# Performance work log

Measured on AMD Instinct MI355X. Metric: run time of the kernel, lower is better.

The kernel has to match this reference:

```python
import jax, jax.numpy as jnp
import numpy as np

B, S, D = 2, 2048, 4096
H, KV, HD = 32, 8, 128
THETA = 10000.0


def rotate_half(x):
    x1, x2 = x[..., : HD // 2], x[..., HD // 2 :]
    return jnp.concatenate((-x2, x1), axis=-1)


def setup_inputs() -> dict:
    key = jax.random.key(0)
    ks = jax.random.split(key, 8)
    s = 1.0 / np.sqrt(D)
    return {
        "hidden_states": jax.random.normal(ks[0], (B, S, D), jnp.float32),
        "modality_indicators": jax.random.randint(ks[1], (B, S), 0, 2, jnp.int64 if jax.config.jax_enable_x64 else jnp.int32),
        "position_ids": jnp.arange(S, dtype=jnp.int32),
        "Wq": jax.random.normal(ks[2], (D, H * HD), jnp.float32) * s,
        "Wk0": jax.random.normal(ks[3], (D, KV * HD), jnp.float32) * s,
        "Wk1": jax.random.normal(ks[4], (D, KV * HD), jnp.float32) * s,
        "Wv0": jax.random.normal(ks[5], (D, KV * HD), jnp.float32) * s,
        "Wv1": jax.random.normal(ks[6], (D, KV * HD), jnp.float32) * s,
        "Wo": jax.random.normal(ks[7], (H * HD, D), jnp.float32) * s,
    }


def reference(hidden_states, modality_indicators, position_ids, Wq, Wk0, Wk1, Wv0, Wv1, Wo):
    x = hidden_states
    # Multiway (modality-routed) k/v projections: per-token select between two linears.
    sel = (modality_indicators == 1)[..., None]  # [B,S,1]
    q = x @ Wq                                   # [B,S,H*HD]
    k = jnp.where(sel, x @ Wk1, x @ Wk0)         # [B,S,KV*HD]
    v = jnp.where(sel, x @ Wv1, x @ Wv0)

    q = q.reshape(B, S, H, HD).transpose(0, 2, 1, 3)    # [B,H,S,HD]
    k = k.reshape(B, S, KV, HD).transpose(0, 2, 1, 3)   # [B,KV,S,HD]
    v = v.reshape(B, S, KV, HD).transpose(0, 2, 1, 3)

    # RoPE cache and application (emb = cat(freqs, freqs))
    inv_freq = 1.0 / (THETA ** (jnp.arange(0, HD, 2, dtype=jnp.float32) / HD))
    freqs = position_ids.astype(jnp.float32)[:, None] * inv_freq[None, :]   # [S,HD/2]
    emb = jnp.concatenate((freqs, freqs), axis=-1)                          # [S,HD]
    cos = jnp.cos(emb)[None, None, :, :]                                    # [1,1,S,HD]
    sin = jnp.sin(emb)[None, None, :, :]
    q = q * cos + rotate_half(q) * sin
    k = k * cos + rotate_half(k) * sin

    # GQA: repeat kv heads
    n_rep = H // KV
    k = jnp.repeat(k, n_rep, axis=1)  # [B,H,S,HD]
    v = jnp.repeat(v, n_rep, axis=1)

    scores = jnp.einsum("bhqd,bhkd->bhqk", q, k) / np.sqrt(HD)
    causal = jnp.tril(jnp.ones((S, S), dtype=bool))
    scores = jnp.where(causal[None, None], scores, jnp.finfo(scores.dtype).min)
    attn = jax.nn.softmax(scores, axis=-1)
    ctx = jnp.einsum("bhqk,bhkd->bhqd", attn, v)            # [B,H,S,HD]
    ctx = ctx.transpose(0, 2, 1, 3).reshape(B, S, H * HD)
    return ctx @ Wo
```

## Files before the change

### kernel.cpp

```cpp
#include <hip/hip_runtime.h>

typedef unsigned short u16;
typedef unsigned int   u32;
using bf16x8 = __attribute__((ext_vector_type(8))) __bf16;
using f32x4  = __attribute__((ext_vector_type(4))) float;
using f32x16 = __attribute__((ext_vector_type(16))) float;
using u32x4  = __attribute__((ext_vector_type(4))) unsigned int;
using ushort8 = __attribute__((ext_vector_type(8))) unsigned short;


__device__ __forceinline__ u16 f2bf(float f) {
  u32 u = __builtin_bit_cast(u32, f);
  return (u16)((u + 0x7fffu + ((u >> 16) & 1u)) >> 16);
}
__device__ __forceinline__ float bf2f(u16 h) {
  return __builtin_bit_cast(float, (u32)h << 16);
}
__device__ __forceinline__ f32x4 mfma16(bf16x8 a, bf16x8 b, f32x4 c) {
  return __builtin_amdgcn_mfma_f32_16x16x32_bf16(a, b, c, 0, 0, 0);
}
__device__ __forceinline__ f32x16 mfma32(bf16x8 a, bf16x8 b, f32x16 c) {
  return __builtin_amdgcn_mfma_f32_32x32x16_bf16(a, b, c, 0, 0, 0);
}
__device__ __forceinline__ f32x16 zero16() {
  f32x16 z;
#pragma unroll
  for (int i = 0; i < 16; ++i) z[i] = 0.f;
  return z;
}
__device__ __forceinline__ void g2l16(const void* gp, void* lp) {
  __builtin_amdgcn_global_load_lds(
      (__attribute__((address_space(1))) void*)(void*)gp,
      (__attribute__((address_space(3))) void*)lp, 16, 0, 0);
}

__global__ void k_cvt(const float* __restrict__ in, u16* __restrict__ out, int n4) {
  int i = blockIdx.x * 256 + threadIdx.x;
  if (i >= n4) return;
  float4 v = ((const float4*)in)[i];
  ushort4 o;
  o.x = f2bf(v.x); o.y = f2bf(v.y); o.z = f2bf(v.z); o.w = f2bf(v.w);
  ((ushort4*)out)[i] = o;
}

__device__ __forceinline__ void tcvt_tile(const float* __restrict__ in, u16* __restrict__ out,
                                          int K, int N, int nt, int kt, u16 (*t)[72]) {
  const int n0 = nt * 64, k0 = kt * 64;
  const int tid = threadIdx.x;
  const int r = tid >> 2, c4 = (tid & 3) * 16;
  const float* src = in + (size_t)(k0 + r) * N + n0 + c4;
#pragma unroll
  for (int q = 0; q < 4; ++q) {
    float4 v = *(const float4*)(src + 4 * q);
    t[c4 + 4 * q + 0][r] = f2bf(v.x);
    t[c4 + 4 * q + 1][r] = f2bf(v.y);
    t[c4 + 4 * q + 2][r] = f2bf(v.z);
    t[c4 + 4 * q + 3][r] = f2bf(v.w);
  }
  __syncthreads();
  u16* dst = out + (size_t)(n0 + r) * K + k0 + c4;
#pragma unroll
  for (int hh = 0; hh < 2; ++hh)
    *(ushort8*)(dst + 8 * hh) = *(const ushort8*)(&t[r][c4 + 8 * hh]);
}

__global__ __launch_bounds__(256) void k_tcvt(const float* __restrict__ in, u16* __restrict__ out,
                                              int K, int N) {
  __shared__ u16 t[64][72];
  tcvt_tile(in, out, K, N, blockIdx.x, blockIdx.y, t);
}

__global__ __launch_bounds__(256) void k_tcvt5(const float* __restrict__ Wq, const float* __restrict__ Wk0,
                                               const float* __restrict__ Wv0, const float* __restrict__ Wk1,
                                               const float* __restrict__ Wv1, u16* __restrict__ WqT,
                                               u16* __restrict__ Wkv0T, u16* __restrict__ Wkv1T) {
  __shared__ u16 t[64][72];
  int bid = blockIdx.x;
  if (bid < 4096) {
    tcvt_tile(Wq, WqT, 4096, 4096, bid & 63, bid >> 6, t);
  } else {
    int r = bid - 4096;
    int mat = r >> 10, rr = r & 1023;
    const float* src = (mat == 0) ? Wk0 : (mat == 1) ? Wv0 : (mat == 2) ? Wk1 : Wv1;
    u16* dst = (mat == 0) ? Wkv0T : (mat == 1) ? (Wkv0T + (size_t)1024 * 4096)
                                  : (mat == 2) ? Wkv1T : (Wkv1T + (size_t)1024 * 4096);
    tcvt_tile(src, dst, 4096, 1024, rr & 15, rr >> 4, t);
  }
}

__global__ void k_scan(const int* __restrict__ mod, int* __restrict__ perm, int* __restrict__ meta) {
  __shared__ int ps[1024];
  const int b = blockIdx.x, t = threadIdx.x;
  perm[b * 2304 + t] = -1;
  perm[b * 2304 + 1024 + t] = -1;
  if (t < 256) perm[b * 2304 + 2048 + t] = -1;
  const int i0 = 2 * t, i1 = 2 * t + 1;
  const int f0 = (mod[b * 2048 + i0] != 1) ? 1 : 0;
  const int f1 = (mod[b * 2048 + i1] != 1) ? 1 : 0;
  const int sum = f0 + f1;
  ps[t] = sum;
  __syncthreads();
  for (int off = 1; off < 1024; off <<= 1) {
    int v = (t >= off) ? ps[t - off] : 0;
    __syncthreads();
    ps[t] += v;
    __syncthreads();
  }
  const int total0 = ps[1023];
  const int excl = ps[t] - sum;
  const int nt0 = (total0 + 255) >> 8;
  const int off1 = nt0 * 256;
  const int s0 = f0 ? excl : off1 + (i0 - excl);
  const int s1 = f1 ? (excl + f0) : off1 + (i1 - (excl + f0));
  perm[b * 2304 + s0] = i0;
  perm[b * 2304 + s1] = i1;
  if (t == 0) { meta[b * 2] = total0; meta[b * 2 + 1] = nt0; }
}

#define BARSB() { __builtin_amdgcn_s_barrier(); __builtin_amdgcn_sched_barrier(0); }
#define VMC(N)  asm volatile("s_waitcnt vmcnt(" #N ")" ::: "memory")

#define READ_A(MH, SL) { _Pragma("unroll") for (int mf_ = 0; mf_ < 4; ++mf_) {       \
    const char* a_ = (const char*)lds8 + (SL)*65536 + (MH)*16384 + (arow + mf_*16)*128; \
    afr[mf_][0] = *(const bf16x8*)(a_ + swc0);                                        \
    afr[mf_][1] = *(const bf16x8*)(a_ + swc1); } }

#define READ_B(NH, SL) { _Pragma("unroll") for (int nf_ = 0; nf_ < 2; ++nf_) {       \
    const char* b_ = (const char*)lds8 + (SL)*65536 + 32768 + (NH)*16384 + (brow + nf_*16)*128; \
    bfr[nf_][0] = *(const bf16x8*)(b_ + swc0);                                        \
    bfr[nf_][1] = *(const bf16x8*)(b_ + swc1); } }

#define MM16(MH, NH) { __builtin_amdgcn_s_setprio(1);                                 \
  _Pragma("unroll") for (int mf_ = 0; mf_ < 4; ++mf_)                                 \
    _Pragma("unroll") for (int nf_ = 0; nf_ < 2; ++nf_) {                             \
      acc[MH][mf_][NH][nf_] = mfma16(afr[mf_][0], bfr[nf_][0], acc[MH][mf_][NH][nf_]); \
      acc[MH][mf_][NH][nf_] = mfma16(afr[mf_][1], bfr[nf_][1], acc[MH][mf_][NH][nf_]); } \
  __builtin_amdgcn_s_setprio(0); }

#define STAGE_A(T, MH) { int ts_ = (T) < 64 ? (T) : 63;                               \
    char* d_ = (char*)lds8 + ((T)&1)*65536 + (MH)*16384 + wid*1024;                   \
    g2l16(pA0[MH] + ts_*64, d_); g2l16(pA1[MH] + ts_*64, d_ + 8192); }

#define STAGE_B(T, NH) { int ts_ = (T) < 64 ? (T) : 63;                               \
    char* d_ = (char*)lds8 + ((T)&1)*65536 + 32768 + (NH)*16384 + wid*1024;           \
    g2l16(pB0[NH] + ts_*64, d_); g2l16(pB1[NH] + ts_*64, d_ + 8192); }

#define G8_MAINLOOP()                                                                 \
  STAGE_A(0,0); STAGE_B(0,1); STAGE_A(0,1); STAGE_B(0,0);                             \
  STAGE_A(1,0); STAGE_B(1,1); STAGE_A(1,1);                                           \
  VMC(6); BARSB();                                                                    \
  for (int i_ = 0; i_ < 32; ++i_) {                                                   \
    const int ta_ = 2 * i_;                                                           \
    READ_A(0,0); READ_B(0,0); STAGE_B(ta_+1, 0); BARSB(); MM16(0,0); BARSB();         \
    READ_B(1,0);              STAGE_A(ta_+2, 0); BARSB(); MM16(0,1); BARSB();         \
    READ_A(1,0);              STAGE_B(ta_+2, 1); BARSB(); MM16(1,1); BARSB();         \
    READ_B(0,0);              STAGE_A(ta_+2, 1); BARSB(); MM16(1,0); VMC(4); BARSB(); \
    READ_A(0,1); READ_B(0,1); STAGE_B(ta_+2, 0); BARSB(); MM16(0,0); BARSB();         \
    READ_B(1,1);              STAGE_A(ta_+3, 0); BARSB(); MM16(0,1); BARSB();         \
    READ_A(1,1);              STAGE_B(ta_+3, 1); BARSB(); MM16(1,1); BARSB();         \
    READ_B(0,1);              STAGE_A(ta_+3, 1); BARSB(); MM16(1,0); VMC(4); BARSB(); \
  }

__global__ __launch_bounds__(512, 2) void k_gemm8(const u16* __restrict__ A, const u16* __restrict__ Bt,
                                                  float* __restrict__ Cp) {
  __shared__ u16 lds8[65536];
  const int tid = threadIdx.x, wid = tid >> 6, l = tid & 63, g = l >> 4, li = l & 15;
  const int wr = wid >> 2, wc = wid & 3;
  const int bid = blockIdx.x;
  const int swz = (bid & 7) * 32 + (bid >> 3);
  const int m0 = (swz >> 4) * 256, n0 = (swz & 15) * 256;

  const int swc0 = (g * 16) ^ ((li & 7) << 4);
  const int swc1 = (64 + g * 16) ^ ((li & 7) << 4);
  const int arow = wr * 64 + li;
  const int brow = wc * 32 + li;

  const int l8a = tid * 16, l8b = 8192 + tid * 16;
  const int oa = l8a ^ (((l8a >> 7) & 7) << 4), ob = l8b ^ (((l8b >> 7) & 7) << 4);
  const int rl0 = oa >> 7, cb0 = oa & 127, rl1 = ob >> 7, cb1 = ob & 127;
  const int RA0 = (rl0 >> 6) * 128 + (rl0 & 63), RA1 = (rl1 >> 6) * 128 + (rl1 & 63);
  const int CB0 = (rl0 >> 5) * 64 + (rl0 & 31), CB1 = (rl1 >> 5) * 64 + (rl1 & 31);
  const u16 *pA0[2], *pA1[2], *pB0[2], *pB1[2];
#pragma unroll
  for (int mh = 0; mh < 2; ++mh) {
    pA0[mh] = A + (size_t)(m0 + RA0 + mh * 64) * 4096 + cb0 / 2;
    pA1[mh] = A + (size_t)(m0 + RA1 + mh * 64) * 4096 + cb1 / 2;
    pB0[mh] = Bt + (size_t)(n0 + CB0 + mh * 32) * 4096 + cb0 / 2;
    pB1[mh] = Bt + (size_t)(n0 + CB1 + mh * 32) * 4096 + cb1 / 2;
  }

  bf16x8 afr[4][2], bfr[2][2];
  const f32x4 vzero = {0.f, 0.f, 0.f, 0.f};
  f32x4 acc[2][4][2][2];
#pragma unroll
  for (int a = 0; a < 2; ++a)
#pragma unroll
    for (int b = 0; b < 4; ++b)
#pragma unroll
      for (int c = 0; c < 2; ++c)
#pragma unroll
        for (int d = 0; d < 2; ++d) acc[a][b][c][d] = vzero;

  G8_MAINLOOP();

#pragma unroll
  for (int mh = 0; mh < 2; ++mh)
#pragma unroll
    for (int mf = 0; mf < 4; ++mf)
#pragma unroll
      for (int nh = 0; nh < 2; ++nh)
#pragma unroll
        for (int nf = 0; nf < 2; ++nf)
#pragma unroll
          for (int j = 0; j < 4; ++j) {
            int row = m0 + wr * 128 + mh * 64 + mf * 16 + g * 4 + j;
            int col = n0 + wc * 64 + nh * 32 + nf * 16 + li;
            Cp[(size_t)row * 4096 + col] = acc[mh][mf][nh][nf][j];
          }
}

#define TB16(T, VMLIT, DOSTAGE)                                              \
  {                                                                          \
    asm volatile("s_waitcnt vmcnt(" VMLIT ")" ::: "memory");                 \
    __builtin_amdgcn_s_barrier();                                            \
    __builtin_amdgcn_sched_barrier(0);                                       \
    const u16* base_ = lds + ((T) & 3) * 16384;                              \
    bf16x8 bfr[4], afr[4];                                                   \
    _Pragma("unroll")                                                        \
    for (int nf = 0; nf < 4; ++nf)                                           \
      bfr[nf] = *(const bf16x8*)(base_ + boff + nf * 512);                   \
    _Pragma("unroll")                                                        \
    for (int mf = 0; mf < 4; ++mf)                                           \
      afr[mf] = *(const bf16x8*)(base_ + aoff + mf * 512);                   \
    if (DOSTAGE) stage((T) + 3);                                             \
    __builtin_amdgcn_s_setprio(1);                                           \
    _Pragma("unroll")                                                        \
    for (int mf = 0; mf < 4; ++mf)                                           \
      _Pragma("unroll")                                                      \
      for (int nf = 0; nf < 4; ++nf)                                         \
        acc[mf][nf] = mfma16(afr[mf], bfr[nf], acc[mf][nf]);                 \
    __builtin_amdgcn_s_setprio(0);                                           \
  }

#define LOOP16()                                                             \
  stage(0); stage(1); stage(2);                                              \
  for (int t = 0; t < 125; ++t) TB16(t, "4", true);                          \
  TB16(125, "4", false);                                                     \
  TB16(126, "2", false);                                                     \
  TB16(127, "0", false);

__global__ __launch_bounds__(1024, 4) void k_gemmQKV(const u16* __restrict__ Xb, const u16* __restrict__ WqT,
                                                     const u16* __restrict__ B0, const u16* __restrict__ B1,
                                                     const int* __restrict__ perm, const int* __restrict__ meta,
                                                     u16* __restrict__ Qr, u16* __restrict__ Ksel,
                                                     u16* __restrict__ Vsel) {
  __shared__ u16 lds[4 * 16384];
  const int tid = threadIdx.x, wid = tid >> 6, l = tid & 63, g = l >> 4, li = l & 15;
  const int wr = wid >> 2, wc = wid & 3;
  const int bid = blockIdx.x;
  const bool isQ = bid < 256;

  const int srow = wid * 16 + (l >> 2);
  const int sgg = (l & 3) ^ ((l >> 3) & 3);

  int m0 = 0, n0 = 0, bb = 0, tm = 0;
  const u16 *pA, *pB;
  if (isQ) {
    const int swz = (bid & 7) * 32 + (bid >> 3);
    m0 = (swz >> 4) * 256; n0 = (swz & 15) * 256;
    pA = Xb + (size_t)(m0 + srow) * 4096 + sgg * 8;
    pB = WqT + (size_t)(n0 + srow) * 4096 + sgg * 8;
  } else {
    const int kb = bid - 256;
    const int seg = kb >> 3;
    n0 = (kb & 7) * 256;
    bb = seg / 9; tm = seg % 9;
    const int nt0 = meta[bb * 2 + 1];
    const u16* Bt = (tm >= nt0) ? B1 : B0;
    int t0 = perm[bb * 2304 + tm * 256 + srow];
    if (t0 < 0) t0 = 0;
    pA = Xb + ((size_t)bb * 2048 + t0) * 4096 + sgg * 8;
    pB = Bt + (size_t)(n0 + srow) * 4096 + sgg * 8;
  }

  auto stage = [&](int t) {
    u16* da = (u16*)lds + (t & 3) * 16384 + wid * 512;
    g2l16(pA + t * 32, da);
    g2l16(pB + t * 32, da + 8192);
  };

  const int lsl8 = (g ^ ((li >> 1) & 3)) * 8;
  const int aoff = (wr * 64 + li) * 32 + lsl8;
  const int boff = 8192 + (wc * 64 + li) * 32 + lsl8;

  const f32x4 vzero = {0.f, 0.f, 0.f, 0.f};
  f32x4 acc[4][4];
#pragma unroll
  for (int m = 0; m < 4; ++m)
#pragma unroll
    for (int n = 0; n < 4; ++n) acc[m][n] = vzero;

  LOOP16();

  if (isQ) {
#pragma unroll
    for (int mf = 0; mf < 4; ++mf)
#pragma unroll
      for (int nf = 0; nf < 4; ++nf)
#pragma unroll
        for (int j = 0; j < 4; ++j) {
          int row = m0 + wr * 64 + mf * 16 + g * 4 + j;
          int col = n0 + wc * 64 + nf * 16 + li;
          int b = row >> 11, s = row & 2047, h = col >> 7, d = col & 127;
          Qr[(((size_t)(b * 32 + h)) * 2048 + s) * 128 + d] = f2bf(acc[mf][nf][j]);
        }
  } else {
#pragma unroll
    for (int mf = 0; mf < 4; ++mf)
#pragma unroll
      for (int nf = 0; nf < 4; ++nf)
#pragma unroll
        for (int j = 0; j < 4; ++j) {
          int slot = tm * 256 + wr * 64 + mf * 16 + g * 4 + j;
          int tok = perm[bb * 2304 + slot];
          if (tok >= 0) {
            int col = n0 + wc * 64 + nf * 16 + li;
            int kv = col >> 10, hh = (col >> 7) & 7, d = col & 127;
            u16* dst = (kv ? Vsel : Ksel) + (((size_t)(bb * 8 + hh)) * 2048 + tok) * 128 + d;
            *dst = f2bf(acc[mf][nf][j]);
          }
        }
  }
}

__global__ __launch_bounds__(256) void k_ropekv(u16* __restrict__ Q, const u16* __restrict__ Ks,
                                                const u16* __restrict__ Vs, const int* __restrict__ pos,
                                                u16* __restrict__ Kr, u16* __restrict__ Vt) {
  __shared__ u16 Vl[64][136];
  const int bid = blockIdx.x;
  const int tid = threadIdx.x, l = tid & 63;
  const float invf = expf((float)l * -0.14391156831212787f);
  if (bid < 32768) {
    int row = bid * 4 + (tid >> 6);
    int s = row & 2047;
    u16* p = Q + (size_t)row * 128;
    float x1 = bf2f(p[l]), x2 = bf2f(p[l + 64]);
    float ang = (float)pos[s] * invf;
    float cs = cosf(ang), sn = sinf(ang);
    const float sc = 0.08838834764831845f;
    p[l] = f2bf((x1 * cs - x2 * sn) * sc);
    p[l + 64] = f2bf((x2 * cs + x1 * sn) * sc);
  } else {
    int blk = bid - 32768;
    int st = blk & 31, kvh = (blk >> 5) & 7, b = blk >> 8;
    int s0 = st * 64;
    int wid = tid >> 6;
    size_t slab = (size_t)(b * 8 + kvh) * 2048;
    for (int rr = 0; rr < 16; ++rr) {
      int r = wid * 16 + rr;
      int s = s0 + r;
      const u16* ks = Ks + (slab + s) * 128;
      const u16* vs = Vs + (slab + s) * 128;
      float ang = (float)pos[s] * invf;
      float cs = cosf(ang), sn = sinf(ang);
      float x1 = bf2f(ks[l]), x2 = bf2f(ks[l + 64]);
      u16* kd = Kr + (slab + s) * 128;
      kd[l] = f2bf(x1 * cs - x2 * sn);
      kd[l + 64] = f2bf(x2 * cs + x1 * sn);
      Vl[r][l] = vs[l];
      Vl[r][l + 64] = vs[l + 64];
    }
    __syncthreads();
    int d = tid >> 1, si0 = (tid & 1) * 32;
    u16* vd = Vt + ((size_t)(b * 8 + kvh) * 128 + d) * 2048 + s0 + si0;
#pragma unroll
    for (int k4 = 0; k4 < 8; ++k4) {
      ushort4 o;
      o.x = Vl[si0 + k4 * 4 + 0][d];
      o.y = Vl[si0 + k4 * 4 + 1][d];
      o.z = Vl[si0 + k4 * 4 + 2][d];
      o.w = Vl[si0 + k4 * 4 + 3][d];
      *(ushort4*)(vd + k4 * 4) = o;
    }
  }
}

__global__ __launch_bounds__(256, 2) void k_attn(const u16* __restrict__ Q, const u16* __restrict__ Kr,
                                                 const u16* __restrict__ Vt, u16* __restrict__ ctx) {
  __shared__ u16 Kl[2 * 64 * 128];
  __shared__ u16 Vl[2 * 128 * 64];
  const int id = blockIdx.x;
  const int gkv = id & 15, j = id >> 4;
  const int b = gkv >> 3, kvh = gkv & 7;
  const int h = kvh * 4 + (j & 3);
  const int p = j >> 2;
  const int bh = b * 32 + h;
  const int tid = threadIdx.x, w = tid >> 6, l = tid & 63;
  const int lo5 = l & 31, hi = l >> 5;
  const bool hib = hi != 0;
  const size_t kvslab = (size_t)(b * 8 + kvh) * 2048;
  const u16* Kg = Kr + kvslab * 128;
  const u16* Vg = Vt + kvslab * 128;
  const float L2E = 1.4426950408889634f;

  auto stage = [&](int kt, int bi) {
#pragma unroll
    for (int i = 0; i < 4; ++i) {
      int c = w * 4 + i;
      int slot = c * 1024 + l * 16;
      {
        int row = slot >> 8;
        int inner = (slot & 255) ^ ((row & 15) << 4);
        g2l16((const char*)Kg + kt * 16384 + row * 256 + inner,
              (char*)Kl + bi * 16384 + c * 1024);
      }
      {
        int row = slot >> 7;
        int inner = (slot & 127) ^ ((row & 7) << 4);
        g2l16((const char*)Vg + (size_t)row * 4096 + kt * 128 + inner,
              (char*)Vl + bi * 16384 + c * 1024);
      }
    }
  };

  for (int hf = 0; hf < 2; ++hf) {
    const int qi = hf ? (15 - p) : p;
    const int q0 = qi * 128;
    const int qlane = q0 + w * 32 + lo5;
    const u16* qrow = Q + ((size_t)bh * 2048 + qlane) * 128;
    bf16x8 qf[8];
#pragma unroll
    for (int kk = 0; kk < 8; ++kk) qf[kk] = *(const bf16x8*)(qrow + kk * 16 + hi * 8);

    f32x16 ot[4];
#pragma unroll
    for (int i = 0; i < 4; ++i) ot[i] = zero16();
    float m = -1e30f, ls = 0.f;

    const int nkt = 2 * qi + 2;
    stage(0, 0);
    stage(1, 1);
    for (int kt = 0; kt < nkt; ++kt) {
      if (kt + 1 < nkt) {
        asm volatile("s_waitcnt vmcnt(8)" ::: "memory");
      } else {
        asm volatile("s_waitcnt vmcnt(0)" ::: "memory");
      }
      __builtin_amdgcn_s_barrier();
      __builtin_amdgcn_sched_barrier(0);
      const char* kbase = (const char*)Kl + (kt & 1) * 16384;
      const char* vbase = (const char*)Vl + (kt & 1) * 16384;
      const int ktb = kt * 64;
      if (ktb <= q0 + w * 32 + 31) {
        f32x16 st[2];
        st[0] = zero16(); st[1] = zero16();
#pragma unroll
        for (int kk = 0; kk < 8; ++kk) {
          bf16x8 kfr[2];
#pragma unroll
          for (int mf = 0; mf < 2; ++mf) {
            int row = mf * 32 + lo5;
            kfr[mf] = *(const bf16x8*)(kbase + row * 256 + ((kk * 32 + hi * 16) ^ ((row & 15) << 4)));
          }
          __builtin_amdgcn_s_setprio(1);
          st[0] = mfma32(kfr[0], qf[kk], st[0]);
          st[1] = mfma32(kfr[1], qf[kk], st[1]);
          __builtin_amdgcn_s_setprio(0);
        }
        if (ktb + 63 > q0 + w * 32) {
#pragma unroll
          for (int mf = 0; mf < 2; ++mf)
#pragma unroll
            for (int r = 0; r < 16; ++r) {
              int kg = ktb + mf * 32 + (r & 3) + 8 * (r >> 2) + 4 * hi;
              if (kg > qlane) st[mf][r] = -3.0e38f;
            }
        }
        float t[16];
#pragma unroll
        for (int r = 0; r < 16; ++r) t[r] = fmaxf(st[0][r], st[1][r]);
#pragma unroll
        for (int s = 8; s >= 1; s >>= 1)
#pragma unroll
          for (int r = 0; r < s; ++r) t[r] = fmaxf(t[r], t[r + s]);
        float pmax = fmaxf(t[0], __shfl_xor(t[0], 32));
        if (!__all(pmax <= m + 8.f)) {
          float nm = fmaxf(m, pmax);
          float resc = exp2f((m - nm) * L2E);
          m = nm;
          ls *= resc;
#pragma unroll
          for (int i = 0; i < 4; ++i)
#pragma unroll
            for (int r = 0; r < 16; ++r) ot[i][r] *= resc;
        }
#pragma unroll
        for (int mf = 0; mf < 2; ++mf)
#pragma unroll
          for (int r = 0; r < 16; ++r) st[mf][r] = exp2f((st[mf][r] - m) * L2E);
        float u[16];
#pragma unroll
        for (int r = 0; r < 16; ++r) u[r] = st[0][r] + st[1][r];
#pragma unroll
        for (int s = 8; s >= 1; s >>= 1)
#pragma unroll
          for (int r = 0; r < s; ++r) u[r] += u[r + s];
        ls += u[0] + __shfl_xor(u[0], 32);
        u32 pkv[16];
#pragma unroll
        for (int mf = 0; mf < 2; ++mf)
#pragma unroll
          for (int tt = 0; tt < 8; ++tt) {
            u32 r;
            asm("v_cvt_pk_bf16_f32 %0, %1, %2" : "=v"(r) : "v"(st[mf][2 * tt]), "v"(st[mf][2 * tt + 1]));
            pkv[mf * 8 + tt] = r;
          }
        bf16x8 pfrag[4];
#pragma unroll
        for (int kk = 0; kk < 4; ++kk) {
          int c = (kk >> 1) * 8 + (kk & 1) * 4;
          u32 m0 = hib ? pkv[c + 2] : pkv[c + 0];
          u32 m1 = hib ? pkv[c + 3] : pkv[c + 1];
          u32 s0 = hib ? pkv[c + 0] : pkv[c + 2];
          u32 s1 = hib ? pkv[c + 1] : pkv[c + 3];
          u32 r0 = (u32)__shfl_xor((int)s0, 32);
          u32 r1 = (u32)__shfl_xor((int)s1, 32);
          u32x4 wv = {hib ? r0 : m0, hib ? r1 : m1, hib ? m0 : r0, hib ? m1 : r1};
          pfrag[kk] = __builtin_bit_cast(bf16x8, wv);
        }
#pragma unroll
        for (int mfV = 0; mfV < 4; ++mfV) {
          int row = mfV * 32 + lo5;
          const char* vb = vbase + row * 128;
          int sw = (row & 7) << 4;
          bf16x8 vf[4];
#pragma unroll
          for (int kk = 0; kk < 4; ++kk)
            vf[kk] = *(const bf16x8*)(vb + ((kk * 32 + hi * 16) ^ sw));
          __builtin_amdgcn_s_setprio(1);
#pragma unroll
          for (int kk = 0; kk < 4; ++kk) ot[mfV] = mfma32(vf[kk], pfrag[kk], ot[mfV]);
          __builtin_amdgcn_s_setprio(0);
        }
      }
      __builtin_amdgcn_s_barrier();
      if (kt + 2 < nkt) stage(kt + 2, kt & 1);
    }
    float inv = 1.0f / ls;
    u16* crow = ctx + ((size_t)(b * 2048) + qlane) * 4096 + h * 128;
#pragma unroll
    for (int mfV = 0; mfV < 4; ++mfV)
#pragma unroll
      for (int rq = 0; rq < 4; ++rq) {
        ushort4 o4;
        o4.x = f2bf(ot[mfV][rq * 4 + 0] * inv);
        o4.y = f2bf(ot[mfV][rq * 4 + 1] * inv);
        o4.z = f2bf(ot[mfV][rq * 4 + 2] * inv);
        o4.w = f2bf(ot[mfV][rq * 4 + 3] * inv);
        *(ushort4*)(crow + mfV * 32 + rq * 8 + hi * 4) = o4;
      }
  }
}

extern "C" void kernel_launch(void* const* d_in, const int* in_sizes, int n_in,
                              void* d_out, int out_size, void* d_ws, size_t ws_size,
                              hipStream_t stream) {
  (void)in_sizes; (void)n_in; (void)out_size; (void)ws_size;
  const float* X   = (const float*)d_in[0];
  const int*   mod = (const int*)d_in[1];
  const int*   pos = (const int*)d_in[2];
  const float* Wq  = (const float*)d_in[3];
  const float* Wk0 = (const float*)d_in[4];
  const float* Wk1 = (const float*)d_in[5];
  const float* Wv0 = (const float*)d_in[6];
  const float* Wv1 = (const float*)d_in[7];
  const float* Wo  = (const float*)d_in[8];
  float* out = (float*)d_out;

  u16* p = (u16*)d_ws;
  auto take = [&](size_t n) { u16* r = p; p += n; return r; };
  u16* Xb    = take(16777216);
  u16* WqT   = take(16777216);
  u16* WoT   = take(16777216);
  u16* Wkv0T = take(8388608);
  u16* Wkv1T = take(8388608);
  u16* Qr    = take(16777216);
  u16* Ksel  = take(4194304);
  u16* Vsel  = take(4194304);
  int* perm  = (int*)take(9216);
  int* meta  = (int*)take(64);
  u16* Kr  = WqT;
  u16* Vtr = WqT + 4194304;
  u16* ctx = Xb;

  k_cvt<<<dim3(16384), 256, 0, stream>>>(X, Xb, 4194304);
  k_scan<<<dim3(2), 1024, 0, stream>>>(mod, perm, meta);
  k_tcvt5<<<dim3(8192), 256, 0, stream>>>(Wq, Wk0, Wv0, Wk1, Wv1, WqT, Wkv0T, Wkv1T);

  k_gemmQKV<<<dim3(400), 1024, 0, stream>>>(Xb, WqT, Wkv0T, Wkv1T, perm, meta, Qr, Ksel, Vsel);

  k_ropekv<<<dim3(33280), 256, 0, stream>>>(Qr, Ksel, Vsel, pos, Kr, Vtr);

  k_attn<<<dim3(512), 256, 0, stream>>>(Qr, Kr, Vtr, ctx);

  k_tcvt<<<dim3(64, 64), 256, 0, stream>>>(Wo, WoT, 4096, 4096);

  k_gemm8<<<dim3(256), 512, 0, stream>>>(ctx, WoT, out);
}
```

Measured before the change: 540.5 us.

## Merge prep kernels, precompute RoPE table, and fuse Q RoPE into attention

The X conversion, weight transposes (now including Wo), the modality scan and a new cos/sin table are folded into one k_prep launch. The scan is rewritten to 256 threads, each handling 8 tokens. Q RoPE and scaling move into the attention kernel at Q-fragment load time, which removes a full read-modify-write pass over Q. K RoPE reads from the precomputed table instead of calling cosf and sinf per element. The cost is extra table loads in attention and a larger, more divergent prep kernel.

```diff
diff --git a/kernel.cpp b/kernel.cpp
--- a/kernel.cpp
+++ b/kernel.cpp
@@ -34,15 +34,6 @@
       (__attribute__((address_space(3))) void*)lp, 16, 0, 0);
 }
 
-__global__ void k_cvt(const float* __restrict__ in, u16* __restrict__ out, int n4) {
-  int i = blockIdx.x * 256 + threadIdx.x;
-  if (i >= n4) return;
-  float4 v = ((const float4*)in)[i];
-  ushort4 o;
-  o.x = f2bf(v.x); o.y = f2bf(v.y); o.z = f2bf(v.z); o.w = f2bf(v.w);
-  ((ushort4*)out)[i] = o;
-}
-
 __device__ __forceinline__ void tcvt_tile(const float* __restrict__ in, u16* __restrict__ out,
                                           int K, int N, int nt, int kt, u16 (*t)[72]) {
   const int n0 = nt * 64, k0 = kt * 64;
@@ -64,57 +55,78 @@
     *(ushort8*)(dst + 8 * hh) = *(const ushort8*)(&t[r][c4 + 8 * hh]);
 }
 
-__global__ __launch_bounds__(256) void k_tcvt(const float* __restrict__ in, u16* __restrict__ out,
-                                              int K, int N) {
+__global__ __launch_bounds__(256) void k_prep(const float* __restrict__ X,
+                                              const float* __restrict__ Wq, const float* __restrict__ Wk0,
+                                              const float* __restrict__ Wv0, const float* __restrict__ Wk1,
+                                              const float* __restrict__ Wv1, const float* __restrict__ Wo,
+                                              const int* __restrict__ mod, const int* __restrict__ pos,
+                                              u16* __restrict__ Xb, u16* __restrict__ WqT,
+                                              u16* __restrict__ Wkv0T, u16* __restrict__ Wkv1T,
+                                              u16* __restrict__ WoT, float2* __restrict__ tab,
+                                              int* __restrict__ perm, int* __restrict__ meta) {
   __shared__ u16 t[64][72];
-  tcvt_tile(in, out, K, N, blockIdx.x, blockIdx.y, t);
-}
-
-__global__ __launch_bounds__(256) void k_tcvt5(const float* __restrict__ Wq, const float* __restrict__ Wk0,
-                                               const float* __restrict__ Wv0, const float* __restrict__ Wk1,
-                                               const float* __restrict__ Wv1, u16* __restrict__ WqT,
-                                               u16* __restrict__ Wkv0T, u16* __restrict__ Wkv1T) {
-  __shared__ u16 t[64][72];
-  int bid = blockIdx.x;
-  if (bid < 4096) {
-    tcvt_tile(Wq, WqT, 4096, 4096, bid & 63, bid >> 6, t);
+  __shared__ int ps[256];
+  const int bid = blockIdx.x, tid = threadIdx.x;
+  if (bid < 16384) {
+    int i = bid * 256 + tid;
+    float4 v = ((const float4*)X)[i];
+    ushort4 o;
+    o.x = f2bf(v.x); o.y = f2bf(v.y); o.z = f2bf(v.z); o.w = f2bf(v.w);
+    ((ushort4*)Xb)[i] = o;
+  } else if (bid < 24576) {
+    int r = bid - 16384;
+    if (r < 4096) {
+      tcvt_tile(Wq, WqT, 4096, 4096, r & 63, r >> 6, t);
+    } else {
+      r -= 4096;
+      int mat = r >> 10, rr = r & 1023;
+      const float* src = (mat == 0) ? Wk0 : (mat == 1) ? Wv0 : (mat == 2) ? Wk1 : Wv1;
+      u16* dst = (mat == 0) ? Wkv0T : (mat == 1) ? (Wkv0T + (size_t)1024 * 4096)
+                                    : (mat == 2) ? Wkv1T : (Wkv1T + (size_t)1024 * 4096);
+      tcvt_tile(src, dst, 4096, 1024, rr & 15, rr >> 4, t);
+    }
+  } else if (bid < 28672) {
+    int r = bid - 24576;
+    tcvt_tile(Wo, WoT, 4096, 4096, r & 63, r >> 6, t);
+  } else if (bid < 29184) {
+    int idx = (bid - 28672) * 256 + tid;
+    int s = idx >> 6, f = idx & 63;
+    float ang = (float)pos[s] * expf((float)f * -0.14391156831212787f);
+    tab[idx] = make_float2(cosf(ang), sinf(ang));
   } else {
-    int r = bid - 4096;
-    int mat = r >> 10, rr = r & 1023;
-    const float* src = (mat == 0) ? Wk0 : (mat == 1) ? Wv0 : (mat == 2) ? Wk1 : Wv1;
-    u16* dst = (mat == 0) ? Wkv0T : (mat == 1) ? (Wkv0T + (size_t)1024 * 4096)
-                                  : (mat == 2) ? Wkv1T : (Wkv1T + (size_t)1024 * 4096);
-    tcvt_tile(src, dst, 4096, 1024, rr & 15, rr >> 4, t);
-  }
-}
-
-__global__ void k_scan(const int* __restrict__ mod, int* __restrict__ perm, int* __restrict__ meta) {
-  __shared__ int ps[1024];
-  const int b = blockIdx.x, t = threadIdx.x;
-  perm[b * 2304 + t] = -1;
-  perm[b * 2304 + 1024 + t] = -1;
-  if (t < 256) perm[b * 2304 + 2048 + t] = -1;
-  const int i0 = 2 * t, i1 = 2 * t + 1;
-  const int f0 = (mod[b * 2048 + i0] != 1) ? 1 : 0;
-  const int f1 = (mod[b * 2048 + i1] != 1) ? 1 : 0;
-  const int sum = f0 + f1;
-  ps[t] = sum;
-  __syncthreads();
-  for (int off = 1; off < 1024; off <<= 1) {
-    int v = (t >= off) ? ps[t - off] : 0;
+    const int b = bid - 29184;
+#pragma unroll
+    for (int i = 0; i < 9; ++i) perm[b * 2304 + i * 256 + tid] = -1;
+    int f[8], loc = 0;
+#pragma unroll
+    for (int i = 0; i < 8; ++i) {
+      f[i] = (mod[b * 2048 + tid * 8 + i] != 1) ? 1 : 0;
+      loc += f[i];
+    }
+    ps[tid] = loc;
     __syncthreads();
-    ps[t] += v;
-    __syncthreads();
-  }
-  const int total0 = ps[1023];
-  const int excl = ps[t] - sum;
-  const int nt0 = (total0 + 255) >> 8;
-  const int off1 = nt0 * 256;
-  const int s0 = f0 ? excl : off1 + (i0 - excl);
-  const int s1 = f1 ? (excl + f0) : off1 + (i1 - (excl + f0));
-  perm[b * 2304 + s0] = i0;
-  perm[b * 2304 + s1] = i1;
-  if (t == 0) { meta[b * 2] = total0; meta[b * 2 + 1] = nt0; }
+    for (int off = 1; off < 256; off <<= 1) {
+      int v = (tid >= off) ? ps[tid - off] : 0;
+      __syncthreads();
+      ps[tid] += v;
+      __syncthreads();
+    }
+    const int total0 = ps[255];
+    int c0 = ps[tid] - loc;
+    const int nt0 = (total0 + 255) >> 8;
+    const int off1 = nt0 * 256;
+#pragma unroll
+    for (int i = 0; i < 8; ++i) {
+      int idx = tid * 8 + i;
+      if (f[i]) {
+        perm[b * 2304 + c0] = idx;
+        ++c0;
+      } else {
+        perm[b * 2304 + off1 + idx - c0] = idx;
+      }
+    }
+    if (tid == 0) { meta[b * 2] = total0; meta[b * 2 + 1] = nt0; }
+  }
 }
 
 #define BARSB() { __builtin_amdgcn_s_barrier(); __builtin_amdgcn_sched_barrier(0); }
@@ -333,60 +345,45 @@
   }
 }
 
-__global__ __launch_bounds__(256) void k_ropekv(u16* __restrict__ Q, const u16* __restrict__ Ks,
-                                                const u16* __restrict__ Vs, const int* __restrict__ pos,
+__global__ __launch_bounds__(256) void k_kvprep(const u16* __restrict__ Ks, const u16* __restrict__ Vs,
+                                                const float2* __restrict__ tab,
                                                 u16* __restrict__ Kr, u16* __restrict__ Vt) {
   __shared__ u16 Vl[64][136];
-  const int bid = blockIdx.x;
-  const int tid = threadIdx.x, l = tid & 63;
-  const float invf = expf((float)l * -0.14391156831212787f);
-  if (bid < 32768) {
-    int row = bid * 4 + (tid >> 6);
-    int s = row & 2047;
-    u16* p = Q + (size_t)row * 128;
-    float x1 = bf2f(p[l]), x2 = bf2f(p[l + 64]);
-    float ang = (float)pos[s] * invf;
-    float cs = cosf(ang), sn = sinf(ang);
-    const float sc = 0.08838834764831845f;
-    p[l] = f2bf((x1 * cs - x2 * sn) * sc);
-    p[l + 64] = f2bf((x2 * cs + x1 * sn) * sc);
-  } else {
-    int blk = bid - 32768;
-    int st = blk & 31, kvh = (blk >> 5) & 7, b = blk >> 8;
-    int s0 = st * 64;
-    int wid = tid >> 6;
-    size_t slab = (size_t)(b * 8 + kvh) * 2048;
-    for (int rr = 0; rr < 16; ++rr) {
-      int r = wid * 16 + rr;
-      int s = s0 + r;
-      const u16* ks = Ks + (slab + s) * 128;
-      const u16* vs = Vs + (slab + s) * 128;
-      float ang = (float)pos[s] * invf;
-      float cs = cosf(ang), sn = sinf(ang);
-      float x1 = bf2f(ks[l]), x2 = bf2f(ks[l + 64]);
-      u16* kd = Kr + (slab + s) * 128;
-      kd[l] = f2bf(x1 * cs - x2 * sn);
-      kd[l + 64] = f2bf(x2 * cs + x1 * sn);
-      Vl[r][l] = vs[l];
-      Vl[r][l + 64] = vs[l + 64];
-    }
-    __syncthreads();
-    int d = tid >> 1, si0 = (tid & 1) * 32;
-    u16* vd = Vt + ((size_t)(b * 8 + kvh) * 128 + d) * 2048 + s0 + si0;
-#pragma unroll
-    for (int k4 = 0; k4 < 8; ++k4) {
-      ushort4 o;
-      o.x = Vl[si0 + k4 * 4 + 0][d];
-      o.y = Vl[si0 + k4 * 4 + 1][d];
-      o.z = Vl[si0 + k4 * 4 + 2][d];
-      o.w = Vl[si0 + k4 * 4 + 3][d];
-      *(ushort4*)(vd + k4 * 4) = o;
-    }
+  int blk = blockIdx.x;
+  int st = blk & 31, kvh = (blk >> 5) & 7, b = blk >> 8;
+  int s0 = st * 64;
+  int tid = threadIdx.x, wid = tid >> 6, l = tid & 63;
+  size_t slab = (size_t)(b * 8 + kvh) * 2048;
+  for (int rr = 0; rr < 16; ++rr) {
+    int r = wid * 16 + rr;
+    int s = s0 + r;
+    const u16* ks = Ks + (slab + s) * 128;
+    const u16* vs = Vs + (slab + s) * 128;
+    float2 cs2 = tab[(size_t)s * 64 + l];
+    float x1 = bf2f(ks[l]), x2 = bf2f(ks[l + 64]);
+    u16* kd = Kr + (slab + s) * 128;
+    kd[l] = f2bf(x1 * cs2.x - x2 * cs2.y);
+    kd[l + 64] = f2bf(x2 * cs2.x + x1 * cs2.y);
+    Vl[r][l] = vs[l];
+    Vl[r][l + 64] = vs[l + 64];
+  }
+  __syncthreads();
+  int d = tid >> 1, si0 = (tid & 1) * 32;
+  u16* vd = Vt + ((size_t)(b * 8 + kvh) * 128 + d) * 2048 + s0 + si0;
+#pragma unroll
+  for (int k4 = 0; k4 < 8; ++k4) {
+    ushort4 o;
+    o.x = Vl[si0 + k4 * 4 + 0][d];
+    o.y = Vl[si0 + k4 * 4 + 1][d];
+    o.z = Vl[si0 + k4 * 4 + 2][d];
+    o.w = Vl[si0 + k4 * 4 + 3][d];
+    *(ushort4*)(vd + k4 * 4) = o;
   }
 }
 
 __global__ __launch_bounds__(256, 2) void k_attn(const u16* __restrict__ Q, const u16* __restrict__ Kr,
-                                                 const u16* __restrict__ Vt, u16* __restrict__ ctx) {
+                                                 const u16* __restrict__ Vt, const float2* __restrict__ tab,
+                                                 u16* __restrict__ ctx) {
   __shared__ u16 Kl[2 * 64 * 128];
   __shared__ u16 Vl[2 * 128 * 64];
   const int id = blockIdx.x;
@@ -431,6 +428,19 @@
     bf16x8 qf[8];
 #pragma unroll
     for (int kk = 0; kk < 8; ++kk) qf[kk] = *(const bf16x8*)(qrow + kk * 16 + hi * 8);
+    {
+      const float2* trow = tab + (size_t)qlane * 64;
+      const float sc = 0.08838834764831845f;
+#pragma unroll
+      for (int kk = 0; kk < 4; ++kk)
+#pragma unroll
+        for (int e = 0; e < 8; ++e) {
+          float2 cs2 = trow[kk * 16 + hi * 8 + e];
+          float x1 = (float)qf[kk][e], x2 = (float)qf[kk + 4][e];
+          qf[kk][e]     = (__bf16)((x1 * cs2.x - x2 * cs2.y) * sc);
+          qf[kk + 4][e] = (__bf16)((x2 * cs2.x + x1 * cs2.y) * sc);
+        }
+    }
 
     f32x16 ot[4];
 #pragma unroll
@@ -587,23 +597,21 @@
   u16* Qr    = take(16777216);
   u16* Ksel  = take(4194304);
   u16* Vsel  = take(4194304);
+  float2* tab = (float2*)take(524288);
   int* perm  = (int*)take(9216);
   int* meta  = (int*)take(64);
   u16* Kr  = WqT;
   u16* Vtr = WqT + 4194304;
   u16* ctx = Xb;
 
-  k_cvt<<<dim3(16384), 256, 0, stream>>>(X, Xb, 4194304);
-  k_scan<<<dim3(2), 1024, 0, stream>>>(mod, perm, meta);
-  k_tcvt5<<<dim3(8192), 256, 0, stream>>>(Wq, Wk0, Wv0, Wk1, Wv1, WqT, Wkv0T, Wkv1T);
+  k_prep<<<dim3(29186), 256, 0, stream>>>(X, Wq, Wk0, Wv0, Wk1, Wv1, Wo, mod, pos,
+                                          Xb, WqT, Wkv0T, Wkv1T, WoT, tab, perm, meta);
 
   k_gemmQKV<<<dim3(400), 1024, 0, stream>>>(Xb, WqT, Wkv0T, Wkv1T, perm, meta, Qr, Ksel, Vsel);
 
-  k_ropekv<<<dim3(33280), 256, 0, stream>>>(Qr, Ksel, Vsel, pos, Kr, Vtr);
-
-  k_attn<<<dim3(512), 256, 0, stream>>>(Qr, Kr, Vtr, ctx);
-
-  k_tcvt<<<dim3(64, 64), 256, 0, stream>>>(Wo, WoT, 4096, 4096);
+  k_kvprep<<<dim3(512), 256, 0, stream>>>(Ksel, Vsel, tab, Kr, Vtr);
+
+  k_attn<<<dim3(512), 256, 0, stream>>>(Qr, Kr, Vtr, tab, ctx);
 
   k_gemm8<<<dim3(256), 512, 0, stream>>>(ctx, WoT, out);
 }
```

Measured after the change: 515.6 us. 1.05x faster.
